# Kernel tuning notes

Hardware: AMD Instinct MI355X
Metric: run time of the kernel (lower is better)

The kernel has to match this reference:

```python
import jax, jax.numpy as jnp
import numpy as np
import math

N, C3, T = 32, 192, 2048  # C3 = 3 * head_dim

def setup_inputs() -> dict:
    key = jax.random.key(0)
    qkv = jax.random.normal(key, (N, C3, T), dtype=jnp.float32)
    return {"qkv": qkv}

def reference(qkv):
    ch = qkv.shape[1] // 3
    q, k, v = jnp.split(qkv, 3, axis=1)              # each [N, C, T]
    scale = 1.0 / math.sqrt(math.sqrt(ch))           # applied to both q and k
    # [N, T, T] attention scores
    weight = jnp.einsum('bct,bcs->bts', q * scale, k * scale)
    weight = jax.nn.softmax(weight.astype(jnp.float32), axis=-1).astype(qkv.dtype)
    # [N, C, T] output
    return jnp.einsum('bts,bcs->bct', weight, v)
```

## Files before the change

### kernel.cpp

```cpp
#include <hip/hip_runtime.h>

#define T_DIM 2048
#define D_DIM 64
#define NB 32

#define QT_OFF 0
#define KB_OFF 4194304
#define VB_OFF 8388608

typedef _Float16 half8 __attribute__((ext_vector_type(8)));
typedef _Float16 half4 __attribute__((ext_vector_type(4)));
typedef float f32x16 __attribute__((ext_vector_type(16)));
typedef float f32x4 __attribute__((ext_vector_type(4)));

#define ZERO16 (f32x16){0.f,0.f,0.f,0.f,0.f,0.f,0.f,0.f,0.f,0.f,0.f,0.f,0.f,0.f,0.f,0.f}

__global__ __launch_bounds__(256) void prepass(const float* __restrict__ qkv,
                                               _Float16* __restrict__ ws) {
  const int ttile = blockIdx.x;
  const int b = blockIdx.y;
  const int type = blockIdx.z;
  const int t0 = ttile * 64;
  __shared__ float Ls[64][65];

  const int tid = threadIdx.x;
  const int cc = tid >> 4;
  const int tt = (tid & 15) << 2;
  const float QS = 0.125f * 1.4426950408889634f;
  const float* src = qkv + ((size_t)b * 192 + type * 64) * T_DIM;
#pragma unroll
  for (int p = 0; p < 4; ++p) {
    const int c = p * 16 + cc;
    float4 v = *(const float4*)&src[(size_t)c * T_DIM + t0 + tt];
    if (type == 0) { v.x *= QS; v.y *= QS; v.z *= QS; v.w *= QS; }
    Ls[c][tt] = v.x; Ls[c][tt + 1] = v.y; Ls[c][tt + 2] = v.z; Ls[c][tt + 3] = v.w;
  }
  __syncthreads();

  if (type == 0) {
    const int t = tid >> 2, cg = (tid & 3) * 16;
    half8 h0, h1;
#pragma unroll
    for (int j = 0; j < 8; ++j) h0[j] = (_Float16)Ls[cg + j][t];
#pragma unroll
    for (int j = 0; j < 8; ++j) h1[j] = (_Float16)Ls[cg + 8 + j][t];
    _Float16* dst = ws + QT_OFF + ((size_t)b * T_DIM + t0 + t) * 64 + cg;
    *(half8*)dst = h0;
    *(half8*)(dst + 8) = h1;
  } else if (type == 1) {
    const int f = tid >> 6, h = (tid >> 5) & 1, s31 = tid & 31;
#pragma unroll
    for (int sbl = 0; sbl < 2; ++sbl) {
      const int sb = (t0 >> 5) + sbl;
      half8 hv;
#pragma unroll
      for (int j = 0; j < 8; ++j) hv[j] = (_Float16)Ls[f * 16 + h * 8 + j][sbl * 32 + s31];
      _Float16* dst = ws + KB_OFF + ((size_t)b * 64 + sb) * 2048 + f * 512 + h * 256 + s31 * 8;
      *(half8*)dst = hv;
    }
  } else {
#pragma unroll
    for (int p = 0; p < 2; ++p) {
      const int g = p * 256 + tid;
      const int sgl = g >> 6, c = g & 63;
      half8 hv;
#pragma unroll
      for (int j = 0; j < 8; ++j) hv[j] = (_Float16)Ls[c][sgl * 8 + j];
      _Float16* dst = ws + VB_OFF + (((size_t)b * 256 + (t0 >> 3) + sgl) * 64 + c) * 8;
      *(half8*)dst = hv;
    }
  }
}

static __device__ __forceinline__ half4 shflx32(half4 x) {
  int2 i = __builtin_bit_cast(int2, x);
  i.x = __shfl_xor(i.x, 32);
  i.y = __shfl_xor(i.y, 32);
  return __builtin_bit_cast(half4, i);
}
static __device__ __forceinline__ half8 cat4(half4 lo, half4 hi) {
  half8 r;
  r[0] = lo[0]; r[1] = lo[1]; r[2] = lo[2]; r[3] = lo[3];
  r[4] = hi[0]; r[5] = hi[1]; r[6] = hi[2]; r[7] = hi[3];
  return r;
}

__global__ __launch_bounds__(256, 2) void qkv_main(const _Float16* __restrict__ ws,
                                                   float* __restrict__ out) {
  const int tid = threadIdx.x;
  const int wave = tid >> 6, lane = tid & 63;
  const int l31 = lane & 31, h = lane >> 5;
  const int b = blockIdx.x & 31;
  const int qg = blockIdx.x >> 5;
  const int t0 = qg * 128 + wave * 32;

  __shared__ _Float16 kv[2][4096];

  const _Float16* Qt = ws + QT_OFF;
  const _Float16* kbase = ws + KB_OFF + (size_t)b * 131072;
  const _Float16* vbase = ws + VB_OFF + (size_t)b * 131072;

  const _Float16* qp = Qt + ((size_t)b * T_DIM + t0 + l31) * 64 + h * 8;
  half8 bq[4];
#pragma unroll
  for (int f = 0; f < 4; ++f) bq[f] = *(const half8*)(qp + f * 16);

  const f32x16 fz = ZERO16;
  f32x16 o0 = ZERO16, o1 = ZERO16;
  float lp = 0.f;

  {
    half8 gk = *(const half8*)(kbase + tid * 8);
    half8 gv = *(const half8*)(vbase + tid * 8);
    *(half8*)&kv[0][tid * 8] = gk;
    *(half8*)&kv[0][2048 + tid * 8] = gv;
  }

  const int koff = lane * 8;
  const int voff = h * 512 + l31 * 8;

  for (int sb = 0; sb < 64; ++sb) {
    const int cur = sb & 1;
    __syncthreads();

    const int sn = (sb + 1 < 64) ? sb + 1 : 63;
    half8 gk = *(const half8*)(kbase + (size_t)sn * 2048 + tid * 8);
    half8 gv = *(const half8*)(vbase + (size_t)sn * 2048 + tid * 8);

    const _Float16* sK = &kv[cur][0];
    const _Float16* sV = &kv[cur][2048];
    half8 ak0 = *(const half8*)&sK[koff];
    half8 ak1 = *(const half8*)&sK[koff + 512];
    half8 ak2 = *(const half8*)&sK[koff + 1024];
    half8 ak3 = *(const half8*)&sK[koff + 1536];
    half8 bv0 = *(const half8*)&sV[voff];
    half8 bv1 = *(const half8*)&sV[voff + 256];
    half8 bv2 = *(const half8*)&sV[voff + 1024];
    half8 bv3 = *(const half8*)&sV[voff + 1280];

    f32x16 s;
    s = __builtin_amdgcn_mfma_f32_32x32x16_f16(ak0, bq[0], fz, 0, 0, 0);
    s = __builtin_amdgcn_mfma_f32_32x32x16_f16(ak1, bq[1], s, 0, 0, 0);
    s = __builtin_amdgcn_mfma_f32_32x32x16_f16(ak2, bq[2], s, 0, 0, 0);
    s = __builtin_amdgcn_mfma_f32_32x32x16_f16(ak3, bq[3], s, 0, 0, 0);

    half4 ap[4];
#pragma unroll
    for (int g = 0; g < 4; ++g) {
      const float e0 = __builtin_amdgcn_exp2f(s[4 * g + 0]);
      const float e1 = __builtin_amdgcn_exp2f(s[4 * g + 1]);
      const float e2 = __builtin_amdgcn_exp2f(s[4 * g + 2]);
      const float e3 = __builtin_amdgcn_exp2f(s[4 * g + 3]);
      lp += (e0 + e1) + (e2 + e3);
      ap[g] = (half4){(_Float16)e0, (_Float16)e1, (_Float16)e2, (_Float16)e3};
    }

    const half4 xs0 = h ? ap[0] : ap[1];
    const half4 ot0 = shflx32(xs0);
    const half8 A0 = cat4(h ? ot0 : ap[0], h ? ap[1] : ot0);
    const half4 xs1 = h ? ap[2] : ap[3];
    const half4 ot1 = shflx32(xs1);
    const half8 A1 = cat4(h ? ot1 : ap[2], h ? ap[3] : ot1);

    o0 = __builtin_amdgcn_mfma_f32_32x32x16_f16(A0, bv0, o0, 0, 0, 0);
    o1 = __builtin_amdgcn_mfma_f32_32x32x16_f16(A0, bv1, o1, 0, 0, 0);
    o0 = __builtin_amdgcn_mfma_f32_32x32x16_f16(A1, bv2, o0, 0, 0, 0);
    o1 = __builtin_amdgcn_mfma_f32_32x32x16_f16(A1, bv3, o1, 0, 0, 0);

    *(half8*)&kv[cur ^ 1][tid * 8] = gk;
    *(half8*)&kv[cur ^ 1][2048 + tid * 8] = gv;
  }

  const float lf = lp + __shfl_xor(lp, 32);
  const float linv = 1.0f / lf;
  float* ob = out + (size_t)b * D_DIM * T_DIM;
#pragma unroll
  for (int g = 0; g < 4; ++g) {
    f32x4 r0, r1;
#pragma unroll
    for (int j = 0; j < 4; ++j) {
      const float il = __shfl(linv, g * 8 + h * 4 + j);
      r0[j] = o0[g * 4 + j] * il;
      r1[j] = o1[g * 4 + j] * il;
    }
    const int q = t0 + g * 8 + h * 4;
    *(f32x4*)&ob[(size_t)l31 * T_DIM + q] = r0;
    *(f32x4*)&ob[(size_t)(32 + l31) * T_DIM + q] = r1;
  }
}

extern "C" void kernel_launch(void* const* d_in, const int* in_sizes, int n_in,
                              void* d_out, int out_size, void* d_ws, size_t ws_size,
                              hipStream_t stream) {
  const float* qkv = (const float*)d_in[0];
  float* out = (float*)d_out;
  _Float16* ws = (_Float16*)d_ws;
  hipLaunchKernelGGL(prepass, dim3(32, 32, 3), dim3(256), 0, stream, qkv, ws);
  hipLaunchKernelGGL(qkv_main, dim3(512), dim3(256), 0, stream, ws, out);
}
```

Measured before the change: 137.0 us.

## Drop LDS staging; software-pipeline K/V register loads with staggered start and setprio

Removes the shared-memory double buffer and per-iteration block barrier, so each wave loads its K/V fragments straight from global (L2) into registers one step ahead. The loop is restructured so the PV MFMAs of one step and the QK MFMAs of the next run back to back while the exp/softmax of the current tile overlaps the next prefetch. Waves start at staggered key blocks to spread L2 access, and s_setprio raises priority around the MFMA bursts. The cost is that each wave now fetches K/V itself (four times the global/L2 traffic per block) and holds more registers live.

```diff
diff --git a/kernel.cpp b/kernel.cpp
--- a/kernel.cpp
+++ b/kernel.cpp
@@ -93,8 +93,7 @@
   const int b = blockIdx.x & 31;
   const int qg = blockIdx.x >> 5;
   const int t0 = qg * 128 + wave * 32;
-
-  __shared__ _Float16 kv[2][4096];
+  const int s0 = ((wave + qg) & 3) * 16;
 
   const _Float16* Qt = ws + QT_OFF;
   const _Float16* kbase = ws + KB_OFF + (size_t)b * 131072;
@@ -109,41 +108,40 @@
   f32x16 o0 = ZERO16, o1 = ZERO16;
   float lp = 0.f;
 
+  const _Float16* kp = kbase + h * 256 + l31 * 8;
+  const _Float16* vp = vbase + h * 512 + l31 * 8;
+
+  half8 ak0, ak1, ak2, ak3, bv0, bv1, bv2, bv3;
+  half8 kn0, kn1, kn2, kn3, vn0, vn1, vn2, vn3;
   {
-    half8 gk = *(const half8*)(kbase + tid * 8);
-    half8 gv = *(const half8*)(vbase + tid * 8);
-    *(half8*)&kv[0][tid * 8] = gk;
-    *(half8*)&kv[0][2048 + tid * 8] = gv;
-  }
-
-  const int koff = lane * 8;
-  const int voff = h * 512 + l31 * 8;
-
-  for (int sb = 0; sb < 64; ++sb) {
-    const int cur = sb & 1;
-    __syncthreads();
-
-    const int sn = (sb + 1 < 64) ? sb + 1 : 63;
-    half8 gk = *(const half8*)(kbase + (size_t)sn * 2048 + tid * 8);
-    half8 gv = *(const half8*)(vbase + (size_t)sn * 2048 + tid * 8);
-
-    const _Float16* sK = &kv[cur][0];
-    const _Float16* sV = &kv[cur][2048];
-    half8 ak0 = *(const half8*)&sK[koff];
-    half8 ak1 = *(const half8*)&sK[koff + 512];
-    half8 ak2 = *(const half8*)&sK[koff + 1024];
-    half8 ak3 = *(const half8*)&sK[koff + 1536];
-    half8 bv0 = *(const half8*)&sV[voff];
-    half8 bv1 = *(const half8*)&sV[voff + 256];
-    half8 bv2 = *(const half8*)&sV[voff + 1024];
-    half8 bv3 = *(const half8*)&sV[voff + 1280];
-
-    f32x16 s;
-    s = __builtin_amdgcn_mfma_f32_32x32x16_f16(ak0, bq[0], fz, 0, 0, 0);
-    s = __builtin_amdgcn_mfma_f32_32x32x16_f16(ak1, bq[1], s, 0, 0, 0);
-    s = __builtin_amdgcn_mfma_f32_32x32x16_f16(ak2, bq[2], s, 0, 0, 0);
-    s = __builtin_amdgcn_mfma_f32_32x32x16_f16(ak3, bq[3], s, 0, 0, 0);
-
+    const size_t ofc = (size_t)s0 * 2048;
+    ak0 = *(const half8*)(kp + ofc);
+    ak1 = *(const half8*)(kp + ofc + 512);
+    ak2 = *(const half8*)(kp + ofc + 1024);
+    ak3 = *(const half8*)(kp + ofc + 1536);
+    bv0 = *(const half8*)(vp + ofc);
+    bv1 = *(const half8*)(vp + ofc + 256);
+    bv2 = *(const half8*)(vp + ofc + 1024);
+    bv3 = *(const half8*)(vp + ofc + 1280);
+  }
+  f32x16 s;
+  s = __builtin_amdgcn_mfma_f32_32x32x16_f16(ak0, bq[0], fz, 0, 0, 0);
+  s = __builtin_amdgcn_mfma_f32_32x32x16_f16(ak1, bq[1], s, 0, 0, 0);
+  s = __builtin_amdgcn_mfma_f32_32x32x16_f16(ak2, bq[2], s, 0, 0, 0);
+  s = __builtin_amdgcn_mfma_f32_32x32x16_f16(ak3, bq[3], s, 0, 0, 0);
+  {
+    const size_t ofn = (size_t)((s0 + 1) & 63) * 2048;
+    kn0 = *(const half8*)(kp + ofn);
+    kn1 = *(const half8*)(kp + ofn + 512);
+    kn2 = *(const half8*)(kp + ofn + 1024);
+    kn3 = *(const half8*)(kp + ofn + 1536);
+    vn0 = *(const half8*)(vp + ofn);
+    vn1 = *(const half8*)(vp + ofn + 256);
+    vn2 = *(const half8*)(vp + ofn + 1024);
+    vn3 = *(const half8*)(vp + ofn + 1280);
+  }
+  half8 A0, A1;
+  {
     half4 ap[4];
 #pragma unroll
     for (int g = 0; g < 4; ++g) {
@@ -154,22 +152,64 @@
       lp += (e0 + e1) + (e2 + e3);
       ap[g] = (half4){(_Float16)e0, (_Float16)e1, (_Float16)e2, (_Float16)e3};
     }
-
     const half4 xs0 = h ? ap[0] : ap[1];
     const half4 ot0 = shflx32(xs0);
-    const half8 A0 = cat4(h ? ot0 : ap[0], h ? ap[1] : ot0);
+    A0 = cat4(h ? ot0 : ap[0], h ? ap[1] : ot0);
     const half4 xs1 = h ? ap[2] : ap[3];
     const half4 ot1 = shflx32(xs1);
-    const half8 A1 = cat4(h ? ot1 : ap[2], h ? ap[3] : ot1);
-
+    A1 = cat4(h ? ot1 : ap[2], h ? ap[3] : ot1);
+  }
+
+  for (int i = 1; i < 64; ++i) {
+    __builtin_amdgcn_s_setprio(1);
     o0 = __builtin_amdgcn_mfma_f32_32x32x16_f16(A0, bv0, o0, 0, 0, 0);
     o1 = __builtin_amdgcn_mfma_f32_32x32x16_f16(A0, bv1, o1, 0, 0, 0);
     o0 = __builtin_amdgcn_mfma_f32_32x32x16_f16(A1, bv2, o0, 0, 0, 0);
     o1 = __builtin_amdgcn_mfma_f32_32x32x16_f16(A1, bv3, o1, 0, 0, 0);
 
-    *(half8*)&kv[cur ^ 1][tid * 8] = gk;
-    *(half8*)&kv[cur ^ 1][2048 + tid * 8] = gv;
-  }
+    ak0 = kn0; ak1 = kn1; ak2 = kn2; ak3 = kn3;
+    bv0 = vn0; bv1 = vn1; bv2 = vn2; bv3 = vn3;
+
+    s = __builtin_amdgcn_mfma_f32_32x32x16_f16(ak0, bq[0], fz, 0, 0, 0);
+    s = __builtin_amdgcn_mfma_f32_32x32x16_f16(ak1, bq[1], s, 0, 0, 0);
+    s = __builtin_amdgcn_mfma_f32_32x32x16_f16(ak2, bq[2], s, 0, 0, 0);
+    s = __builtin_amdgcn_mfma_f32_32x32x16_f16(ak3, bq[3], s, 0, 0, 0);
+    __builtin_amdgcn_s_setprio(0);
+
+    const size_t ofn = (size_t)((s0 + i + 1) & 63) * 2048;
+    kn0 = *(const half8*)(kp + ofn);
+    kn1 = *(const half8*)(kp + ofn + 512);
+    kn2 = *(const half8*)(kp + ofn + 1024);
+    kn3 = *(const half8*)(kp + ofn + 1536);
+    vn0 = *(const half8*)(vp + ofn);
+    vn1 = *(const half8*)(vp + ofn + 256);
+    vn2 = *(const half8*)(vp + ofn + 1024);
+    vn3 = *(const half8*)(vp + ofn + 1280);
+
+    half4 ap[4];
+#pragma unroll
+    for (int g = 0; g < 4; ++g) {
+      const float e0 = __builtin_amdgcn_exp2f(s[4 * g + 0]);
+      const float e1 = __builtin_amdgcn_exp2f(s[4 * g + 1]);
+      const float e2 = __builtin_amdgcn_exp2f(s[4 * g + 2]);
+      const float e3 = __builtin_amdgcn_exp2f(s[4 * g + 3]);
+      lp += (e0 + e1) + (e2 + e3);
+      ap[g] = (half4){(_Float16)e0, (_Float16)e1, (_Float16)e2, (_Float16)e3};
+    }
+    const half4 xs0 = h ? ap[0] : ap[1];
+    const half4 ot0 = shflx32(xs0);
+    A0 = cat4(h ? ot0 : ap[0], h ? ap[1] : ot0);
+    const half4 xs1 = h ? ap[2] : ap[3];
+    const half4 ot1 = shflx32(xs1);
+    A1 = cat4(h ? ot1 : ap[2], h ? ap[3] : ot1);
+  }
+
+  __builtin_amdgcn_s_setprio(1);
+  o0 = __builtin_amdgcn_mfma_f32_32x32x16_f16(A0, bv0, o0, 0, 0, 0);
+  o1 = __builtin_amdgcn_mfma_f32_32x32x16_f16(A0, bv1, o1, 0, 0, 0);
+  o0 = __builtin_amdgcn_mfma_f32_32x32x16_f16(A1, bv2, o0, 0, 0, 0);
+  o1 = __builtin_amdgcn_mfma_f32_32x32x16_f16(A1, bv3, o1, 0, 0, 0);
+  __builtin_amdgcn_s_setprio(0);
 
   const float lf = lp + __shfl_xor(lp, 32);
   const float linv = 1.0f / lf;
```

Result: slower. 141.8 us (+3.5%).
